# Kernel tuning notes

Measured on AMD Instinct MI355X. Metric: run time of the kernel, lower is better.

## Reference

```python
import jax, jax.numpy as jnp
import numpy as np

EPS = 1e-6

def _rms_norm(t):
    rms = jnp.sqrt(jnp.mean(t * t, axis=-1, keepdims=True) + EPS)
    return t / rms

def setup_inputs() -> dict:
    key = jax.random.key(0)
    ks = jax.random.split(key, 7)
    B, N, IN, OUT, R = 16, 2048, 256, 256, 64
    x = jax.random.normal(ks[0], (B, N, 4, IN), dtype=jnp.float32)
    # factors initialized as random normals (orthogonal init in torch; distribution irrelevant for math)
    scale = 1.0 / np.sqrt(IN)
    factor_tl = jax.random.normal(ks[1], (N, R, IN), dtype=jnp.float32) * scale
    factor_tr = jax.random.normal(ks[2], (N, R, IN), dtype=jnp.float32) * scale
    factor_bl = jax.random.normal(ks[3], (N, R, IN), dtype=jnp.float32) * scale
    factor_br = jax.random.normal(ks[4], (N, R, IN), dtype=jnp.float32) * scale
    factor_out = jax.random.normal(ks[5], (N, R, OUT), dtype=jnp.float32) * (1.0 / np.sqrt(R))
    gain = jnp.ones((N, 1), dtype=jnp.float32)
    return {"x": x, "factor_tl": factor_tl, "factor_tr": factor_tr,
            "factor_bl": factor_bl, "factor_br": factor_br,
            "factor_out": factor_out, "gain": gain}

def reference(x, factor_tl, factor_tr, factor_bl, factor_br, factor_out, gain):
    # per-node batched projections: [B,N,in] x [N,R,in] -> [B,N,R]
    p_tl = _rms_norm(jnp.einsum('bni,nri->bnr', x[:, :, 0, :], factor_tl))
    p_tr = _rms_norm(jnp.einsum('bni,nri->bnr', x[:, :, 1, :], factor_tr))
    p_bl = _rms_norm(jnp.einsum('bni,nri->bnr', x[:, :, 2, :], factor_bl))
    p_br = _rms_norm(jnp.einsum('bni,nri->bnr', x[:, :, 3, :], factor_br))
    merged = p_tl * p_tr * p_bl * p_br * gain[None, :, :]  # [B,N,R]
    out = jnp.einsum('bnr,nro->bno', merged, factor_out)   # [B,N,out]
    # use_residual=True, in_dim == out_dim -> identity residual projection
    return out + jnp.mean(x, axis=2)
```

## Files before the change

kernel.cpp:

```cpp
#include <hip/hip_runtime.h>
#include <math.h>


#define WAITVM(NLIT) asm volatile("s_waitcnt vmcnt(" #NLIT ") lgkmcnt(0)" ::: "memory")
#define LGKM0()      asm volatile("s_waitcnt lgkmcnt(0)" ::: "memory")
#define BARRIER()    __builtin_amdgcn_s_barrier()

__device__ __forceinline__ void g2l16(const float* g, float* l) {
  __builtin_amdgcn_global_load_lds(
      (const __attribute__((address_space(1))) void*)g,
      (__attribute__((address_space(3))) void*)l, 16, 0, 0);
}

#define NN 2048

__global__ __launch_bounds__(512, 2) void cpquad_kernel(
    const float* __restrict__ x,
    const float* __restrict__ ftl, const float* __restrict__ ftr,
    const float* __restrict__ fbl, const float* __restrict__ fbr,
    const float* __restrict__ fout, const float* __restrict__ gain,
    float* __restrict__ out) {

  alignas(16) __shared__ float s_fb[3 * 4096];
  alignas(16) __shared__ float s_xs[2 * 1024];
  alignas(16) __shared__ float s_ps[4096];
  __shared__ float s_rr[64];

  const int t = threadIdx.x, lane = t & 63, wid = t >> 6;
  const int n = blockIdx.x;
  const float gn = gain[n];

  const int q0 = wid >> 1;
  const int r0 = (wid & 1) * 32 + (lane >> 2);
  const float* fq0 = (q0 == 0) ? ftl : ((q0 == 1) ? ftr : ((q0 == 2) ? fbl : fbr));
  const float* ss0 =
      fq0 + ((size_t)n * 64 + r0) * 256 + (((lane & 3) ^ ((lane >> 3) & 3)) << 2);
  const int c2 = wid * 16 + (lane >> 2);
  const float* xsrc =
      x + (((size_t)(c2 >> 2) * NN + n) * 4 + (c2 & 3)) * 256 + (lane & 3) * 4;
  const float* osrc = fout + (size_t)n * 16384 + wid * 512 + lane * 4;

  auto ISSUE_SLAB = [&](int s) {
    float* d = s_fb + (s % 3) * 4096 + wid * 512;
    g2l16(ss0 + s * 16, d);
    g2l16(ss0 + 4096 + s * 16, d + 256);
  };
  auto ISSUE_X = [&](int p) {
    if (wid < 4) g2l16(xsrc + p * 16, s_xs + (p & 1) * 1024 + wid * 256);
  };
  auto ISSUE_FO = [&](int h) {
    float* d = s_fb + ((16 + h) % 3) * 4096 + wid * 512;
    g2l16(osrc + h * 4096, d);
    g2l16(osrc + h * 4096 + 256, d + 256);
  };

  ISSUE_X(0);
  ISSUE_SLAB(0);
  ISSUE_SLAB(1);

  const int iseg = t & 3;
  const int bh   = (t >> 2) & 1;
  const int rg   = (t >> 3) & 15;
  const int qq   = t >> 7;
  const int fsl  = (iseg ^ ((rg >> 1) & 3)) << 2;

  float acc[4][8];
#pragma unroll
  for (int k = 0; k < 4; ++k)
#pragma unroll
    for (int b = 0; b < 8; ++b) acc[k][b] = 0.0f;

#pragma unroll 2
  for (int p = 0; p < 16; ++p) {
    if (p < 15) ISSUE_X(p + 1);
    if (p < 14) ISSUE_SLAB(p + 2); else ISSUE_FO(p - 14);
    if (p < 15) {
      if (wid < 4) { WAITVM(5); } else { WAITVM(4); }
    } else {
      WAITVM(4);
    }
    BARRIER();

    const float* fb = s_fb + (p % 3) * 4096 + qq * 1024;
    const float* xb = s_xs + (p & 1) * 1024;
    float4 fv[4];
#pragma unroll
    for (int k = 0; k < 4; ++k)
      fv[k] = *(const float4*)(fb + (k * 16 + rg) * 16 + fsl);
#pragma unroll
    for (int h2 = 0; h2 < 2; ++h2) {
      float4 xv[4];
#pragma unroll
      for (int bb = 0; bb < 4; ++bb)
        xv[bb] = *(const float4*)(xb + ((bh * 8 + h2 * 4 + bb) * 4 + qq) * 16 + (iseg << 2));
#pragma unroll
      for (int k = 0; k < 4; ++k)
#pragma unroll
        for (int bb = 0; bb < 4; ++bb) {
          acc[k][h2 * 4 + bb] = fmaf(fv[k].x, xv[bb].x, acc[k][h2 * 4 + bb]);
          acc[k][h2 * 4 + bb] = fmaf(fv[k].y, xv[bb].y, acc[k][h2 * 4 + bb]);
          acc[k][h2 * 4 + bb] = fmaf(fv[k].z, xv[bb].z, acc[k][h2 * 4 + bb]);
          acc[k][h2 * 4 + bb] = fmaf(fv[k].w, xv[bb].w, acc[k][h2 * 4 + bb]);
        }
    }
    LGKM0();
    BARRIER();
  }

  ISSUE_FO(2);

#pragma unroll
  for (int k = 0; k < 4; ++k)
#pragma unroll
    for (int b = 0; b < 8; ++b) {
      float v = acc[k][b];
      v += __shfl_xor(v, 1);
      v += __shfl_xor(v, 2);
      acc[k][b] = v;
    }
#pragma unroll
  for (int k = 0; k < 4; ++k) {
    if (iseg == k) {
#pragma unroll
      for (int b = 0; b < 8; ++b)
        s_ps[qq * 1024 + (bh * 8 + b) * 64 + k * 16 + rg] = acc[k][b];
    }
  }
  LGKM0(); BARRIER();

#pragma unroll
  for (int j = 0; j < 8; ++j) {
    const int row = wid * 8 + j;
    const float v = s_ps[row * 64 + lane];
    float ssum = v * v;
#pragma unroll
    for (int d = 1; d < 64; d <<= 1) ssum += __shfl_xor(ssum, d);
    if (lane == 0) s_rr[row] = 1.0f / sqrtf(ssum * (1.0f / 64.0f) + 1e-6f);
  }
  LGKM0(); BARRIER();

#pragma unroll
  for (int e0 = 0; e0 < 2; ++e0) {
    const int e = t + e0 * 512;
    const int b = e >> 6, r = e & 63;
    float m = gn;
#pragma unroll
    for (int q = 0; q < 4; ++q) m *= s_ps[q * 1024 + b * 64 + r] * s_rr[q * 16 + b];
    s_ps[b * 64 + r] = m;
  }

  float oa[2][4] = {{0.f, 0.f, 0.f, 0.f}, {0.f, 0.f, 0.f, 0.f}};
#pragma unroll
  for (int h = 0; h < 4; ++h) {
    if (h == 0)      { WAITVM(4); }
    else if (h == 1) { WAITVM(4); }
    else if (h == 2) { WAITVM(2); }
    else             { WAITVM(0); }
    BARRIER();
    const float* fsp = s_fb + ((16 + h) % 3) * 4096;
#pragma unroll
    for (int rr = 0; rr < 16; ++rr) {
      const float4 f4 = *(const float4*)(fsp + rr * 256 + (lane << 2));
      const float m0 = s_ps[(wid * 2 + 0) * 64 + h * 16 + rr];
      const float m1 = s_ps[(wid * 2 + 1) * 64 + h * 16 + rr];
      oa[0][0] = fmaf(m0, f4.x, oa[0][0]); oa[0][1] = fmaf(m0, f4.y, oa[0][1]);
      oa[0][2] = fmaf(m0, f4.z, oa[0][2]); oa[0][3] = fmaf(m0, f4.w, oa[0][3]);
      oa[1][0] = fmaf(m1, f4.x, oa[1][0]); oa[1][1] = fmaf(m1, f4.y, oa[1][1]);
      oa[1][2] = fmaf(m1, f4.z, oa[1][2]); oa[1][3] = fmaf(m1, f4.w, oa[1][3]);
    }
    if (h == 0) {
      BARRIER();
      ISSUE_FO(3);
    }
  }

#pragma unroll
  for (int bb = 0; bb < 2; ++bb) {
    const int b = wid * 2 + bb;
    const float* xe = x + (((size_t)b * NN + n) * 4) * 256 + (lane << 2);
    float4 x0 = *(const float4*)(xe);
    float4 x1 = *(const float4*)(xe + 256);
    float4 x2 = *(const float4*)(xe + 512);
    float4 x3 = *(const float4*)(xe + 768);
    float4 o4;
    o4.x = oa[bb][0] + 0.25f * (x0.x + x1.x + x2.x + x3.x);
    o4.y = oa[bb][1] + 0.25f * (x0.y + x1.y + x2.y + x3.y);
    o4.z = oa[bb][2] + 0.25f * (x0.z + x1.z + x2.z + x3.z);
    o4.w = oa[bb][3] + 0.25f * (x0.w + x1.w + x2.w + x3.w);
    *(float4*)(out + ((size_t)b * NN + n) * 256 + (lane << 2)) = o4;
  }
}

extern "C" void kernel_launch(void* const* d_in, const int* in_sizes, int n_in,
                              void* d_out, int out_size, void* d_ws, size_t ws_size,
                              hipStream_t stream) {
  const float* x   = (const float*)d_in[0];
  const float* ftl = (const float*)d_in[1];
  const float* ftr = (const float*)d_in[2];
  const float* fbl = (const float*)d_in[3];
  const float* fbr = (const float*)d_in[4];
  const float* fo  = (const float*)d_in[5];
  const float* gn  = (const float*)d_in[6];
  float* o = (float*)d_out;
  cpquad_kernel<<<dim3(NN), dim3(512), 0, stream>>>(x, ftl, ftr, fbl, fbr, fo, gn, o);
}
```

Baseline: 200.2 us.

## Process four nodes per persistent block with cross-node prefetch pipelining

Each block now loops over four consecutive nodes. The next node's first x and factor slabs are prefetched while the current node's output GEMV runs, which hides the pipeline fill at each node boundary. The residual x loads are issued early and the merged weights come through readlane instead of LDS reads, with the vmcnt waits retuned to match. In exchange the grid shrinks to 512 blocks, which may underfill 256 CUs at 2 blocks per CU, and the hand-counted waitcnt values are fragile.

```diff
diff --git a/kernel.cpp b/kernel.cpp
--- a/kernel.cpp
+++ b/kernel.cpp
@@ -5,6 +5,7 @@
 #define WAITVM(NLIT) asm volatile("s_waitcnt vmcnt(" #NLIT ") lgkmcnt(0)" ::: "memory")
 #define LGKM0()      asm volatile("s_waitcnt lgkmcnt(0)" ::: "memory")
 #define BARRIER()    __builtin_amdgcn_s_barrier()
+#define MEMFENCE()   asm volatile("" ::: "memory")
 
 __device__ __forceinline__ void g2l16(const float* g, float* l) {
   __builtin_amdgcn_global_load_lds(
@@ -13,6 +14,7 @@
 }
 
 #define NN 2048
+#define ITERS 4
 
 __global__ __launch_bounds__(512, 2) void cpquad_kernel(
     const float* __restrict__ x,
@@ -27,18 +29,17 @@
   __shared__ float s_rr[64];
 
   const int t = threadIdx.x, lane = t & 63, wid = t >> 6;
-  const int n = blockIdx.x;
-  const float gn = gain[n];
+  const int n0 = blockIdx.x * ITERS;
 
   const int q0 = wid >> 1;
   const int r0 = (wid & 1) * 32 + (lane >> 2);
   const float* fq0 = (q0 == 0) ? ftl : ((q0 == 1) ? ftr : ((q0 == 2) ? fbl : fbr));
   const float* ss0 =
-      fq0 + ((size_t)n * 64 + r0) * 256 + (((lane & 3) ^ ((lane >> 3) & 3)) << 2);
+      fq0 + ((size_t)n0 * 64 + r0) * 256 + (((lane & 3) ^ ((lane >> 3) & 3)) << 2);
   const int c2 = wid * 16 + (lane >> 2);
   const float* xsrc =
-      x + (((size_t)(c2 >> 2) * NN + n) * 4 + (c2 & 3)) * 256 + (lane & 3) * 4;
-  const float* osrc = fout + (size_t)n * 16384 + wid * 512 + lane * 4;
+      x + (((size_t)(c2 >> 2) * NN + n0) * 4 + (c2 & 3)) * 256 + (lane & 3) * 4;
+  const float* osrc = fout + (size_t)n0 * 16384 + wid * 512 + lane * 4;
 
   auto ISSUE_SLAB = [&](int s) {
     float* d = s_fb + (s % 3) * 4096 + wid * 512;
@@ -54,140 +55,165 @@
     g2l16(osrc + h * 4096 + 256, d + 256);
   };
 
-  ISSUE_X(0);
-  ISSUE_SLAB(0);
-  ISSUE_SLAB(1);
-
   const int iseg = t & 3;
   const int bh   = (t >> 2) & 1;
   const int rg   = (t >> 3) & 15;
   const int qq   = t >> 7;
   const int fsl  = (iseg ^ ((rg >> 1) & 3)) << 2;
 
-  float acc[4][8];
-#pragma unroll
-  for (int k = 0; k < 4; ++k)
-#pragma unroll
-    for (int b = 0; b < 8; ++b) acc[k][b] = 0.0f;
+#pragma unroll 1
+  for (int it = 0; it < ITERS; ++it) {
+    const int n = n0 + it;
+    const float gn = gain[n];
+
+    if (it == 0) {
+      ISSUE_X(0);
+      ISSUE_SLAB(0);
+      ISSUE_SLAB(1);
+    }
+
+    float acc[4][8];
+#pragma unroll
+    for (int k = 0; k < 4; ++k)
+#pragma unroll
+      for (int b = 0; b < 8; ++b) acc[k][b] = 0.0f;
 
 #pragma unroll 2
-  for (int p = 0; p < 16; ++p) {
-    if (p < 15) ISSUE_X(p + 1);
-    if (p < 14) ISSUE_SLAB(p + 2); else ISSUE_FO(p - 14);
-    if (p < 15) {
-      if (wid < 4) { WAITVM(5); } else { WAITVM(4); }
-    } else {
-      WAITVM(4);
-    }
+    for (int p = 0; p < 16; ++p) {
+      if (p < 15) ISSUE_X(p + 1);
+      if (p < 14) ISSUE_SLAB(p + 2); else ISSUE_FO(p - 14);
+      if (p < 15) {
+        if (wid < 4) { WAITVM(5); } else { WAITVM(4); }
+      } else {
+        WAITVM(4);
+      }
+      BARRIER();
+
+      const float* fb = s_fb + (p % 3) * 4096 + qq * 1024;
+      const float* xb = s_xs + (p & 1) * 1024;
+      float4 fv[4];
+#pragma unroll
+      for (int k = 0; k < 4; ++k)
+        fv[k] = *(const float4*)(fb + (k * 16 + rg) * 16 + fsl);
+#pragma unroll
+      for (int h2 = 0; h2 < 2; ++h2) {
+        float4 xv[4];
+#pragma unroll
+        for (int bb = 0; bb < 4; ++bb)
+          xv[bb] = *(const float4*)(xb + ((bh * 8 + h2 * 4 + bb) * 4 + qq) * 16 + (iseg << 2));
+#pragma unroll
+        for (int k = 0; k < 4; ++k)
+#pragma unroll
+          for (int bb = 0; bb < 4; ++bb) {
+            acc[k][h2 * 4 + bb] = fmaf(fv[k].x, xv[bb].x, acc[k][h2 * 4 + bb]);
+            acc[k][h2 * 4 + bb] = fmaf(fv[k].y, xv[bb].y, acc[k][h2 * 4 + bb]);
+            acc[k][h2 * 4 + bb] = fmaf(fv[k].z, xv[bb].z, acc[k][h2 * 4 + bb]);
+            acc[k][h2 * 4 + bb] = fmaf(fv[k].w, xv[bb].w, acc[k][h2 * 4 + bb]);
+          }
+      }
+      LGKM0();
+      BARRIER();
+    }
+
+    ISSUE_FO(2);
+    MEMFENCE();
+    float4 xr0[4], xr1[4];
+#pragma unroll
+    for (int q = 0; q < 4; ++q) {
+      xr0[q] = *(const float4*)(x + (((size_t)(wid * 2 + 0) * NN + n) * 4 + q) * 256 + (lane << 2));
+      xr1[q] = *(const float4*)(x + (((size_t)(wid * 2 + 1) * NN + n) * 4 + q) * 256 + (lane << 2));
+    }
+    MEMFENCE();
+
+#pragma unroll
+    for (int k = 0; k < 4; ++k)
+#pragma unroll
+      for (int b = 0; b < 8; ++b) {
+        float v = acc[k][b];
+        v += __shfl_xor(v, 1);
+        v += __shfl_xor(v, 2);
+        acc[k][b] = v;
+      }
+#pragma unroll
+    for (int k = 0; k < 4; ++k) {
+      if (iseg == k) {
+#pragma unroll
+        for (int b = 0; b < 8; ++b)
+          s_ps[qq * 1024 + (bh * 8 + b) * 64 + k * 16 + rg] = acc[k][b];
+      }
+    }
+    LGKM0(); BARRIER();
+
+#pragma unroll
+    for (int j = 0; j < 8; ++j) {
+      const int row = wid * 8 + j;
+      const float v = s_ps[row * 64 + lane];
+      float ssum = v * v;
+#pragma unroll
+      for (int d = 1; d < 64; d <<= 1) ssum += __shfl_xor(ssum, d);
+      if (lane == 0) s_rr[row] = 1.0f / sqrtf(ssum * (1.0f / 64.0f) + 1e-6f);
+    }
+    LGKM0(); BARRIER();
+
+#pragma unroll
+    for (int e0 = 0; e0 < 2; ++e0) {
+      const int e = t + e0 * 512;
+      const int b = e >> 6, r = e & 63;
+      float m = gn;
+#pragma unroll
+      for (int q = 0; q < 4; ++q) m *= s_ps[q * 1024 + b * 64 + r] * s_rr[q * 16 + b];
+      s_ps[b * 64 + r] = m;
+    }
+
+    WAITVM(12); BARRIER();
+    const float mv0 = s_ps[(wid * 2 + 0) * 64 + lane];
+    const float mv1 = s_ps[(wid * 2 + 1) * 64 + lane];
+
+    float oa[2][4] = {{0.f, 0.f, 0.f, 0.f}, {0.f, 0.f, 0.f, 0.f}};
+    auto gemq = [&](int h, const float* fsp) {
+#pragma unroll
+      for (int rr = 0; rr < 16; ++rr) {
+        const float4 f4 = *(const float4*)(fsp + rr * 256 + (lane << 2));
+        const float m0 = __uint_as_float(__builtin_amdgcn_readlane(__float_as_uint(mv0), h * 16 + rr));
+        const float m1 = __uint_as_float(__builtin_amdgcn_readlane(__float_as_uint(mv1), h * 16 + rr));
+        oa[0][0] = fmaf(m0, f4.x, oa[0][0]); oa[0][1] = fmaf(m0, f4.y, oa[0][1]);
+        oa[0][2] = fmaf(m0, f4.z, oa[0][2]); oa[0][3] = fmaf(m0, f4.w, oa[0][3]);
+        oa[1][0] = fmaf(m1, f4.x, oa[1][0]); oa[1][1] = fmaf(m1, f4.y, oa[1][1]);
+        oa[1][2] = fmaf(m1, f4.z, oa[1][2]); oa[1][3] = fmaf(m1, f4.w, oa[1][3]);
+      }
+    };
+
+    gemq(0, s_fb + 1 * 4096);
     BARRIER();
-
-    const float* fb = s_fb + (p % 3) * 4096 + qq * 1024;
-    const float* xb = s_xs + (p & 1) * 1024;
-    float4 fv[4];
-#pragma unroll
-    for (int k = 0; k < 4; ++k)
-      fv[k] = *(const float4*)(fb + (k * 16 + rg) * 16 + fsl);
-#pragma unroll
-    for (int h2 = 0; h2 < 2; ++h2) {
-      float4 xv[4];
-#pragma unroll
-      for (int bb = 0; bb < 4; ++bb)
-        xv[bb] = *(const float4*)(xb + ((bh * 8 + h2 * 4 + bb) * 4 + qq) * 16 + (iseg << 2));
-#pragma unroll
-      for (int k = 0; k < 4; ++k)
-#pragma unroll
-        for (int bb = 0; bb < 4; ++bb) {
-          acc[k][h2 * 4 + bb] = fmaf(fv[k].x, xv[bb].x, acc[k][h2 * 4 + bb]);
-          acc[k][h2 * 4 + bb] = fmaf(fv[k].y, xv[bb].y, acc[k][h2 * 4 + bb]);
-          acc[k][h2 * 4 + bb] = fmaf(fv[k].z, xv[bb].z, acc[k][h2 * 4 + bb]);
-          acc[k][h2 * 4 + bb] = fmaf(fv[k].w, xv[bb].w, acc[k][h2 * 4 + bb]);
-        }
-    }
-    LGKM0();
+    ISSUE_FO(3);
+    WAITVM(12); BARRIER();
+    gemq(1, s_fb + 2 * 4096);
+    WAITVM(10); BARRIER();
+    gemq(2, s_fb + 0 * 4096);
+    WAITVM(0); BARRIER();
+    if (it != ITERS - 1) {
+      ss0 += 16384; xsrc += 1024; osrc += 16384;
+      ISSUE_X(0);
+      ISSUE_SLAB(0);
+    }
+    gemq(3, s_fb + 1 * 4096);
     BARRIER();
-  }
-
-  ISSUE_FO(2);
-
-#pragma unroll
-  for (int k = 0; k < 4; ++k)
-#pragma unroll
-    for (int b = 0; b < 8; ++b) {
-      float v = acc[k][b];
-      v += __shfl_xor(v, 1);
-      v += __shfl_xor(v, 2);
-      acc[k][b] = v;
-    }
-#pragma unroll
-  for (int k = 0; k < 4; ++k) {
-    if (iseg == k) {
-#pragma unroll
-      for (int b = 0; b < 8; ++b)
-        s_ps[qq * 1024 + (bh * 8 + b) * 64 + k * 16 + rg] = acc[k][b];
-    }
-  }
-  LGKM0(); BARRIER();
-
-#pragma unroll
-  for (int j = 0; j < 8; ++j) {
-    const int row = wid * 8 + j;
-    const float v = s_ps[row * 64 + lane];
-    float ssum = v * v;
-#pragma unroll
-    for (int d = 1; d < 64; d <<= 1) ssum += __shfl_xor(ssum, d);
-    if (lane == 0) s_rr[row] = 1.0f / sqrtf(ssum * (1.0f / 64.0f) + 1e-6f);
-  }
-  LGKM0(); BARRIER();
-
-#pragma unroll
-  for (int e0 = 0; e0 < 2; ++e0) {
-    const int e = t + e0 * 512;
-    const int b = e >> 6, r = e & 63;
-    float m = gn;
-#pragma unroll
-    for (int q = 0; q < 4; ++q) m *= s_ps[q * 1024 + b * 64 + r] * s_rr[q * 16 + b];
-    s_ps[b * 64 + r] = m;
-  }
-
-  float oa[2][4] = {{0.f, 0.f, 0.f, 0.f}, {0.f, 0.f, 0.f, 0.f}};
-#pragma unroll
-  for (int h = 0; h < 4; ++h) {
-    if (h == 0)      { WAITVM(4); }
-    else if (h == 1) { WAITVM(4); }
-    else if (h == 2) { WAITVM(2); }
-    else             { WAITVM(0); }
-    BARRIER();
-    const float* fsp = s_fb + ((16 + h) % 3) * 4096;
-#pragma unroll
-    for (int rr = 0; rr < 16; ++rr) {
-      const float4 f4 = *(const float4*)(fsp + rr * 256 + (lane << 2));
-      const float m0 = s_ps[(wid * 2 + 0) * 64 + h * 16 + rr];
-      const float m1 = s_ps[(wid * 2 + 1) * 64 + h * 16 + rr];
-      oa[0][0] = fmaf(m0, f4.x, oa[0][0]); oa[0][1] = fmaf(m0, f4.y, oa[0][1]);
-      oa[0][2] = fmaf(m0, f4.z, oa[0][2]); oa[0][3] = fmaf(m0, f4.w, oa[0][3]);
-      oa[1][0] = fmaf(m1, f4.x, oa[1][0]); oa[1][1] = fmaf(m1, f4.y, oa[1][1]);
-      oa[1][2] = fmaf(m1, f4.z, oa[1][2]); oa[1][3] = fmaf(m1, f4.w, oa[1][3]);
-    }
-    if (h == 0) {
-      BARRIER();
-      ISSUE_FO(3);
-    }
-  }
-
-#pragma unroll
-  for (int bb = 0; bb < 2; ++bb) {
-    const int b = wid * 2 + bb;
-    const float* xe = x + (((size_t)b * NN + n) * 4) * 256 + (lane << 2);
-    float4 x0 = *(const float4*)(xe);
-    float4 x1 = *(const float4*)(xe + 256);
-    float4 x2 = *(const float4*)(xe + 512);
-    float4 x3 = *(const float4*)(xe + 768);
-    float4 o4;
-    o4.x = oa[bb][0] + 0.25f * (x0.x + x1.x + x2.x + x3.x);
-    o4.y = oa[bb][1] + 0.25f * (x0.y + x1.y + x2.y + x3.y);
-    o4.z = oa[bb][2] + 0.25f * (x0.z + x1.z + x2.z + x3.z);
-    o4.w = oa[bb][3] + 0.25f * (x0.w + x1.w + x2.w + x3.w);
-    *(float4*)(out + ((size_t)b * NN + n) * 256 + (lane << 2)) = o4;
+    if (it != ITERS - 1) ISSUE_SLAB(1);
+
+    {
+      const int b0 = wid * 2;
+      float4 o4;
+      o4.x = oa[0][0] + 0.25f * (xr0[0].x + xr0[1].x + xr0[2].x + xr0[3].x);
+      o4.y = oa[0][1] + 0.25f * (xr0[0].y + xr0[1].y + xr0[2].y + xr0[3].y);
+      o4.z = oa[0][2] + 0.25f * (xr0[0].z + xr0[1].z + xr0[2].z + xr0[3].z);
+      o4.w = oa[0][3] + 0.25f * (xr0[0].w + xr0[1].w + xr0[2].w + xr0[3].w);
+      *(float4*)(out + ((size_t)b0 * NN + n) * 256 + (lane << 2)) = o4;
+      o4.x = oa[1][0] + 0.25f * (xr1[0].x + xr1[1].x + xr1[2].x + xr1[3].x);
+      o4.y = oa[1][1] + 0.25f * (xr1[0].y + xr1[1].y + xr1[2].y + xr1[3].y);
+      o4.z = oa[1][2] + 0.25f * (xr1[0].z + xr1[1].z + xr1[2].z + xr1[3].z);
+      o4.w = oa[1][3] + 0.25f * (xr1[0].w + xr1[1].w + xr1[2].w + xr1[3].w);
+      *(float4*)(out + ((size_t)(b0 + 1) * NN + n) * 256 + (lane << 2)) = o4;
+    }
   }
 }
 
@@ -202,5 +228,5 @@
   const float* fo  = (const float*)d_in[5];
   const float* gn  = (const float*)d_in[6];
   float* o = (float*)d_out;
-  cpquad_kernel<<<dim3(NN), dim3(512), 0, stream>>>(x, ftl, ftr, fbl, fbr, fo, gn, o);
+  cpquad_kernel<<<dim3(NN / ITERS), dim3(512), 0, stream>>>(x, ftl, ftr, fbl, fbr, fo, gn, o);
 }
```

New measurement: 371.1 us. 1.85x slower.

## Halve LDS staging slabs to fit three blocks per CU, with deeper pipeline

Applied to the files above, without the earlier changes.

Shrinks the K-slab staged per pipeline step from 16 to 8 floats, which halves the shared-memory ring buffers and lets launch bounds request three 512-thread blocks per CU instead of two. The projection loop now runs 32 narrower steps using float2 reads without the XOR swizzle. The output GEMM streams factor_out in eight 2048-float chunks through the triple buffer, and the merged coefficients come from register readlane rather than LDS reads. This trades more barriers and issue overhead per step for higher occupancy and latency hiding, and it risks register spilling under the tighter launch bound.

```diff
diff --git a/kernel.cpp b/kernel.cpp
--- a/kernel.cpp
+++ b/kernel.cpp
@@ -14,15 +14,15 @@
 
 #define NN 2048
 
-__global__ __launch_bounds__(512, 2) void cpquad_kernel(
+__global__ __launch_bounds__(512, 3) void cpquad_kernel(
     const float* __restrict__ x,
     const float* __restrict__ ftl, const float* __restrict__ ftr,
     const float* __restrict__ fbl, const float* __restrict__ fbr,
     const float* __restrict__ fout, const float* __restrict__ gain,
     float* __restrict__ out) {
 
-  alignas(16) __shared__ float s_fb[3 * 4096];
-  alignas(16) __shared__ float s_xs[2 * 1024];
+  alignas(16) __shared__ float s_fb[3 * 2048];
+  alignas(16) __shared__ float s_xs[2 * 512];
   alignas(16) __shared__ float s_ps[4096];
   __shared__ float s_rr[64];
 
@@ -31,27 +31,22 @@
   const float gn = gain[n];
 
   const int q0 = wid >> 1;
-  const int r0 = (wid & 1) * 32 + (lane >> 2);
+  const int r0 = (wid & 1) * 32 + (lane >> 1);
   const float* fq0 = (q0 == 0) ? ftl : ((q0 == 1) ? ftr : ((q0 == 2) ? fbl : fbr));
-  const float* ss0 =
-      fq0 + ((size_t)n * 64 + r0) * 256 + (((lane & 3) ^ ((lane >> 3) & 3)) << 2);
-  const int c2 = wid * 16 + (lane >> 2);
+  const float* ss0 = fq0 + ((size_t)n * 64 + r0) * 256 + (lane & 1) * 4;
+  const int c2 = wid * 32 + (lane >> 1);
   const float* xsrc =
-      x + (((size_t)(c2 >> 2) * NN + n) * 4 + (c2 & 3)) * 256 + (lane & 3) * 4;
-  const float* osrc = fout + (size_t)n * 16384 + wid * 512 + lane * 4;
+      x + (((size_t)(c2 >> 2) * NN + n) * 4 + (c2 & 3)) * 256 + (lane & 1) * 4;
+  const float* osrc = fout + (size_t)n * 16384 + wid * 256 + lane * 4;
 
   auto ISSUE_SLAB = [&](int s) {
-    float* d = s_fb + (s % 3) * 4096 + wid * 512;
-    g2l16(ss0 + s * 16, d);
-    g2l16(ss0 + 4096 + s * 16, d + 256);
+    g2l16(ss0 + s * 8, s_fb + (s % 3) * 2048 + wid * 256);
   };
   auto ISSUE_X = [&](int p) {
-    if (wid < 4) g2l16(xsrc + p * 16, s_xs + (p & 1) * 1024 + wid * 256);
+    if (wid < 2) g2l16(xsrc + p * 8, s_xs + (p & 1) * 512 + wid * 256);
   };
-  auto ISSUE_FO = [&](int h) {
-    float* d = s_fb + ((16 + h) % 3) * 4096 + wid * 512;
-    g2l16(osrc + h * 4096, d);
-    g2l16(osrc + h * 4096 + 256, d + 256);
+  auto ISSUE_E = [&](int h) {
+    g2l16(osrc + h * 2048, s_fb + ((32 + h) % 3) * 2048 + wid * 256);
   };
 
   ISSUE_X(0);
@@ -62,7 +57,6 @@
   const int bh   = (t >> 2) & 1;
   const int rg   = (t >> 3) & 15;
   const int qq   = t >> 7;
-  const int fsl  = (iseg ^ ((rg >> 1) & 3)) << 2;
 
   float acc[4][8];
 #pragma unroll
@@ -71,43 +65,39 @@
     for (int b = 0; b < 8; ++b) acc[k][b] = 0.0f;
 
 #pragma unroll 2
-  for (int p = 0; p < 16; ++p) {
-    if (p < 15) ISSUE_X(p + 1);
-    if (p < 14) ISSUE_SLAB(p + 2); else ISSUE_FO(p - 14);
-    if (p < 15) {
-      if (wid < 4) { WAITVM(5); } else { WAITVM(4); }
+  for (int p = 0; p < 32; ++p) {
+    if (p < 31) ISSUE_X(p + 1);
+    if (p < 30) ISSUE_SLAB(p + 2); else ISSUE_E(p - 30);
+    if (p < 31) {
+      if (wid < 2) { WAITVM(3); } else { WAITVM(2); }
     } else {
-      WAITVM(4);
-    }
-    BARRIER();
-
-    const float* fb = s_fb + (p % 3) * 4096 + qq * 1024;
-    const float* xb = s_xs + (p & 1) * 1024;
-    float4 fv[4];
+      WAITVM(2);
+    }
+    BARRIER();
+
+    const float* fb = s_fb + (p % 3) * 2048 + qq * 512;
+    const float* xb = s_xs + (p & 1) * 512;
+    float2 fv[4];
 #pragma unroll
     for (int k = 0; k < 4; ++k)
-      fv[k] = *(const float4*)(fb + (k * 16 + rg) * 16 + fsl);
-#pragma unroll
-    for (int h2 = 0; h2 < 2; ++h2) {
-      float4 xv[4];
-#pragma unroll
-      for (int bb = 0; bb < 4; ++bb)
-        xv[bb] = *(const float4*)(xb + ((bh * 8 + h2 * 4 + bb) * 4 + qq) * 16 + (iseg << 2));
-#pragma unroll
-      for (int k = 0; k < 4; ++k)
-#pragma unroll
-        for (int bb = 0; bb < 4; ++bb) {
-          acc[k][h2 * 4 + bb] = fmaf(fv[k].x, xv[bb].x, acc[k][h2 * 4 + bb]);
-          acc[k][h2 * 4 + bb] = fmaf(fv[k].y, xv[bb].y, acc[k][h2 * 4 + bb]);
-          acc[k][h2 * 4 + bb] = fmaf(fv[k].z, xv[bb].z, acc[k][h2 * 4 + bb]);
-          acc[k][h2 * 4 + bb] = fmaf(fv[k].w, xv[bb].w, acc[k][h2 * 4 + bb]);
-        }
+      fv[k] = *(const float2*)(fb + (k * 16 + rg) * 8 + iseg * 2);
+#pragma unroll
+    for (int h2 = 0; h2 < 4; ++h2) {
+      const float2 xv0 = *(const float2*)(xb + ((bh * 8 + h2 * 2 + 0) * 4 + qq) * 8 + iseg * 2);
+      const float2 xv1 = *(const float2*)(xb + ((bh * 8 + h2 * 2 + 1) * 4 + qq) * 8 + iseg * 2);
+#pragma unroll
+      for (int k = 0; k < 4; ++k) {
+        acc[k][h2 * 2 + 0] = fmaf(fv[k].x, xv0.x, acc[k][h2 * 2 + 0]);
+        acc[k][h2 * 2 + 0] = fmaf(fv[k].y, xv0.y, acc[k][h2 * 2 + 0]);
+        acc[k][h2 * 2 + 1] = fmaf(fv[k].x, xv1.x, acc[k][h2 * 2 + 1]);
+        acc[k][h2 * 2 + 1] = fmaf(fv[k].y, xv1.y, acc[k][h2 * 2 + 1]);
+      }
     }
     LGKM0();
     BARRIER();
   }
 
-  ISSUE_FO(2);
+  ISSUE_E(2);
 
 #pragma unroll
   for (int k = 0; k < 4; ++k)
@@ -150,28 +140,32 @@
   }
 
   float oa[2][4] = {{0.f, 0.f, 0.f, 0.f}, {0.f, 0.f, 0.f, 0.f}};
-#pragma unroll
-  for (int h = 0; h < 4; ++h) {
-    if (h == 0)      { WAITVM(4); }
-    else if (h == 1) { WAITVM(4); }
-    else if (h == 2) { WAITVM(2); }
+  float mv0, mv1;
+
+#pragma unroll
+  for (int h = 0; h < 8; ++h) {
+    if (h <= 5)      { WAITVM(2); }
+    else if (h == 6) { WAITVM(1); }
     else             { WAITVM(0); }
     BARRIER();
-    const float* fsp = s_fb + ((16 + h) % 3) * 4096;
-#pragma unroll
-    for (int rr = 0; rr < 16; ++rr) {
+    if (h == 0) {
+      mv0 = s_ps[(wid * 2 + 0) * 64 + lane];
+      mv1 = s_ps[(wid * 2 + 1) * 64 + lane];
+    }
+    const float* fsp = s_fb + ((2 + h) % 3) * 2048;
+#pragma unroll
+    for (int rr = 0; rr < 8; ++rr) {
       const float4 f4 = *(const float4*)(fsp + rr * 256 + (lane << 2));
-      const float m0 = s_ps[(wid * 2 + 0) * 64 + h * 16 + rr];
-      const float m1 = s_ps[(wid * 2 + 1) * 64 + h * 16 + rr];
+      const float m0 = __uint_as_float(__builtin_amdgcn_readlane(__float_as_uint(mv0), h * 8 + rr));
+      const float m1 = __uint_as_float(__builtin_amdgcn_readlane(__float_as_uint(mv1), h * 8 + rr));
       oa[0][0] = fmaf(m0, f4.x, oa[0][0]); oa[0][1] = fmaf(m0, f4.y, oa[0][1]);
       oa[0][2] = fmaf(m0, f4.z, oa[0][2]); oa[0][3] = fmaf(m0, f4.w, oa[0][3]);
       oa[1][0] = fmaf(m1, f4.x, oa[1][0]); oa[1][1] = fmaf(m1, f4.y, oa[1][1]);
       oa[1][2] = fmaf(m1, f4.z, oa[1][2]); oa[1][3] = fmaf(m1, f4.w, oa[1][3]);
     }
-    if (h == 0) {
-      BARRIER();
-      ISSUE_FO(3);
-    }
+    LGKM0();
+    BARRIER();
+    if (h <= 4) ISSUE_E(h + 3);
   }
 
 #pragma unroll
```

New measurement: 245.9 us. +22.8%, slower.

## Replace async LDS pipelining with direct global loads and readlane broadcast

Applied to the files above, without the earlier changes.

Removes the triple-buffered global_load_lds pipeline for the factor and x tiles. The projection loop now reads float4 operands straight from global memory into registers, and the output projection streams factor_out from global, broadcasting merged values with readlane instead of reading them from LDS. This frees most of the shared memory and raises launch bounds to 3 blocks per CU for more occupancy. In exchange it loses explicit prefetch overlap and relies on caches and occupancy to hide global latency, with x and factor loads now duplicated across threads.

```diff
diff --git a/kernel.cpp b/kernel.cpp
--- a/kernel.cpp
+++ b/kernel.cpp
@@ -2,67 +2,30 @@
 #include <math.h>
 
 
-#define WAITVM(NLIT) asm volatile("s_waitcnt vmcnt(" #NLIT ") lgkmcnt(0)" ::: "memory")
-#define LGKM0()      asm volatile("s_waitcnt lgkmcnt(0)" ::: "memory")
-#define BARRIER()    __builtin_amdgcn_s_barrier()
-
-__device__ __forceinline__ void g2l16(const float* g, float* l) {
-  __builtin_amdgcn_global_load_lds(
-      (const __attribute__((address_space(1))) void*)g,
-      (__attribute__((address_space(3))) void*)l, 16, 0, 0);
-}
-
 #define NN 2048
 
-__global__ __launch_bounds__(512, 2) void cpquad_kernel(
+__global__ __launch_bounds__(512, 3) void cpquad_kernel(
     const float* __restrict__ x,
     const float* __restrict__ ftl, const float* __restrict__ ftr,
     const float* __restrict__ fbl, const float* __restrict__ fbr,
     const float* __restrict__ fout, const float* __restrict__ gain,
     float* __restrict__ out) {
 
-  alignas(16) __shared__ float s_fb[3 * 4096];
-  alignas(16) __shared__ float s_xs[2 * 1024];
-  alignas(16) __shared__ float s_ps[4096];
+  __shared__ float s_ps[4096];
   __shared__ float s_rr[64];
 
   const int t = threadIdx.x, lane = t & 63, wid = t >> 6;
   const int n = blockIdx.x;
   const float gn = gain[n];
 
-  const int q0 = wid >> 1;
-  const int r0 = (wid & 1) * 32 + (lane >> 2);
-  const float* fq0 = (q0 == 0) ? ftl : ((q0 == 1) ? ftr : ((q0 == 2) ? fbl : fbr));
-  const float* ss0 =
-      fq0 + ((size_t)n * 64 + r0) * 256 + (((lane & 3) ^ ((lane >> 3) & 3)) << 2);
-  const int c2 = wid * 16 + (lane >> 2);
-  const float* xsrc =
-      x + (((size_t)(c2 >> 2) * NN + n) * 4 + (c2 & 3)) * 256 + (lane & 3) * 4;
-  const float* osrc = fout + (size_t)n * 16384 + wid * 512 + lane * 4;
-
-  auto ISSUE_SLAB = [&](int s) {
-    float* d = s_fb + (s % 3) * 4096 + wid * 512;
-    g2l16(ss0 + s * 16, d);
-    g2l16(ss0 + 4096 + s * 16, d + 256);
-  };
-  auto ISSUE_X = [&](int p) {
-    if (wid < 4) g2l16(xsrc + p * 16, s_xs + (p & 1) * 1024 + wid * 256);
-  };
-  auto ISSUE_FO = [&](int h) {
-    float* d = s_fb + ((16 + h) % 3) * 4096 + wid * 512;
-    g2l16(osrc + h * 4096, d);
-    g2l16(osrc + h * 4096 + 256, d + 256);
-  };
-
-  ISSUE_X(0);
-  ISSUE_SLAB(0);
-  ISSUE_SLAB(1);
-
   const int iseg = t & 3;
   const int bh   = (t >> 2) & 1;
   const int rg   = (t >> 3) & 15;
   const int qq   = t >> 7;
-  const int fsl  = (iseg ^ ((rg >> 1) & 3)) << 2;
+
+  const float* fq0 = (qq == 0) ? ftl : ((qq == 1) ? ftr : ((qq == 2) ? fbl : fbr));
+  const float* fbase = fq0 + ((size_t)n * 64 + rg) * 256 + (iseg << 2);
+  const float* xbase = x + (((size_t)(bh * 8) * NN + n) * 4 + qq) * 256 + (iseg << 2);
 
   float acc[4][8];
 #pragma unroll
@@ -72,27 +35,16 @@
 
 #pragma unroll 2
   for (int p = 0; p < 16; ++p) {
-    if (p < 15) ISSUE_X(p + 1);
-    if (p < 14) ISSUE_SLAB(p + 2); else ISSUE_FO(p - 14);
-    if (p < 15) {
-      if (wid < 4) { WAITVM(5); } else { WAITVM(4); }
-    } else {
-      WAITVM(4);
-    }
-    BARRIER();
-
-    const float* fb = s_fb + (p % 3) * 4096 + qq * 1024;
-    const float* xb = s_xs + (p & 1) * 1024;
     float4 fv[4];
 #pragma unroll
     for (int k = 0; k < 4; ++k)
-      fv[k] = *(const float4*)(fb + (k * 16 + rg) * 16 + fsl);
+      fv[k] = *(const float4*)(fbase + k * 4096 + p * 16);
 #pragma unroll
     for (int h2 = 0; h2 < 2; ++h2) {
       float4 xv[4];
 #pragma unroll
       for (int bb = 0; bb < 4; ++bb)
-        xv[bb] = *(const float4*)(xb + ((bh * 8 + h2 * 4 + bb) * 4 + qq) * 16 + (iseg << 2));
+        xv[bb] = *(const float4*)(xbase + (size_t)(h2 * 4 + bb) * (NN * 1024) + p * 16);
 #pragma unroll
       for (int k = 0; k < 4; ++k)
 #pragma unroll
@@ -103,11 +55,7 @@
           acc[k][h2 * 4 + bb] = fmaf(fv[k].w, xv[bb].w, acc[k][h2 * 4 + bb]);
         }
     }
-    LGKM0();
-    BARRIER();
   }
-
-  ISSUE_FO(2);
 
 #pragma unroll
   for (int k = 0; k < 4; ++k)
@@ -126,7 +74,7 @@
         s_ps[qq * 1024 + (bh * 8 + b) * 64 + k * 16 + rg] = acc[k][b];
     }
   }
-  LGKM0(); BARRIER();
+  __syncthreads();
 
 #pragma unroll
   for (int j = 0; j < 8; ++j) {
@@ -137,7 +85,7 @@
     for (int d = 1; d < 64; d <<= 1) ssum += __shfl_xor(ssum, d);
     if (lane == 0) s_rr[row] = 1.0f / sqrtf(ssum * (1.0f / 64.0f) + 1e-6f);
   }
-  LGKM0(); BARRIER();
+  __syncthreads();
 
 #pragma unroll
   for (int e0 = 0; e0 < 2; ++e0) {
@@ -148,30 +96,22 @@
     for (int q = 0; q < 4; ++q) m *= s_ps[q * 1024 + b * 64 + r] * s_rr[q * 16 + b];
     s_ps[b * 64 + r] = m;
   }
+  __syncthreads();
+
+  const float mv0 = s_ps[(wid * 2 + 0) * 64 + lane];
+  const float mv1 = s_ps[(wid * 2 + 1) * 64 + lane];
+  const float* fo_n = fout + (size_t)n * 16384 + (lane << 2);
 
   float oa[2][4] = {{0.f, 0.f, 0.f, 0.f}, {0.f, 0.f, 0.f, 0.f}};
-#pragma unroll
-  for (int h = 0; h < 4; ++h) {
-    if (h == 0)      { WAITVM(4); }
-    else if (h == 1) { WAITVM(4); }
-    else if (h == 2) { WAITVM(2); }
-    else             { WAITVM(0); }
-    BARRIER();
-    const float* fsp = s_fb + ((16 + h) % 3) * 4096;
-#pragma unroll
-    for (int rr = 0; rr < 16; ++rr) {
-      const float4 f4 = *(const float4*)(fsp + rr * 256 + (lane << 2));
-      const float m0 = s_ps[(wid * 2 + 0) * 64 + h * 16 + rr];
-      const float m1 = s_ps[(wid * 2 + 1) * 64 + h * 16 + rr];
-      oa[0][0] = fmaf(m0, f4.x, oa[0][0]); oa[0][1] = fmaf(m0, f4.y, oa[0][1]);
-      oa[0][2] = fmaf(m0, f4.z, oa[0][2]); oa[0][3] = fmaf(m0, f4.w, oa[0][3]);
-      oa[1][0] = fmaf(m1, f4.x, oa[1][0]); oa[1][1] = fmaf(m1, f4.y, oa[1][1]);
-      oa[1][2] = fmaf(m1, f4.z, oa[1][2]); oa[1][3] = fmaf(m1, f4.w, oa[1][3]);
-    }
-    if (h == 0) {
-      BARRIER();
-      ISSUE_FO(3);
-    }
+#pragma unroll 8
+  for (int rr = 0; rr < 64; ++rr) {
+    const float4 f4 = *(const float4*)(fo_n + rr * 256);
+    const float m0 = __uint_as_float(__builtin_amdgcn_readlane(__float_as_uint(mv0), rr));
+    const float m1 = __uint_as_float(__builtin_amdgcn_readlane(__float_as_uint(mv1), rr));
+    oa[0][0] = fmaf(m0, f4.x, oa[0][0]); oa[0][1] = fmaf(m0, f4.y, oa[0][1]);
+    oa[0][2] = fmaf(m0, f4.z, oa[0][2]); oa[0][3] = fmaf(m0, f4.w, oa[0][3]);
+    oa[1][0] = fmaf(m1, f4.x, oa[1][0]); oa[1][1] = fmaf(m1, f4.y, oa[1][1]);
+    oa[1][2] = fmaf(m1, f4.z, oa[1][2]); oa[1][3] = fmaf(m1, f4.w, oa[1][3]);
   }
 
 #pragma unroll
```

Measured after the change: 251.3 us. 1.26x slower.
